# Performance work log

Hardware: AMD Instinct MI355X
Metric: run time of the kernel (lower is better)

Reference implementation:

```python
import jax, jax.numpy as jnp
import numpy as np

ALPHA = 1.0


def setup_inputs() -> dict:
    key = jax.random.key(0)
    k1, k2 = jax.random.split(key)
    x = jax.random.normal(k1, (131072, 512), dtype=jnp.float32)
    # glorot_uniform-ish small init for cluster centers (K, D)
    limit = np.sqrt(6.0 / (128 + 512)).astype(np.float32)
    clusters = jax.random.uniform(k2, (128, 512), dtype=jnp.float32,
                                  minval=-limit, maxval=limit)
    return {"x": x, "clusters": clusters}


def reference(x, clusters):
    # Squared euclidean distance via matmul decomposition:
    # ||x_i - c_j||^2 = ||x_i||^2 + ||c_j||^2 - 2 x_i . c_j
    # Avoids materializing the (N, K, D) broadcast intermediate.
    x2 = jnp.sum(x * x, axis=1, keepdims=True)            # (N, 1)
    c2 = jnp.sum(clusters * clusters, axis=1)             # (K,)
    cross = jnp.einsum('nd,kd->nk', x, clusters)          # (N, K)
    d2 = jnp.maximum(x2 + c2[None, :] - 2.0 * cross, 0.0)  # (N, K)
    q = 1.0 / (1.0 + d2 / ALPHA)
    q = q ** ((ALPHA + 1.0) / 2.0)
    q = q / jnp.sum(q, axis=1, keepdims=True)             # row-normalize
    return q
```

## Files before the change

### kernel.cpp

```cpp
#include <hip/hip_runtime.h>
#include <hip/hip_bf16.h>

typedef __bf16 bf16x8 __attribute__((ext_vector_type(8)));
typedef float f32x4 __attribute__((ext_vector_type(4)));

__global__ __launch_bounds__(64)
void prep_clusters(const float* __restrict__ c, __bf16* __restrict__ cb,
                   float* __restrict__ c2)
{
    const int row = blockIdx.x;
    const int l = threadIdx.x;
    const float* p = c + row * 512 + l * 8;
    f32x4 u0 = *(const f32x4*)p;
    f32x4 u1 = *(const f32x4*)(p + 4);
    bf16x8 v;
    float s = 0.f;
#pragma unroll
    for (int j = 0; j < 4; ++j) {
        v[j]     = (__bf16)u0[j];
        v[4 + j] = (__bf16)u1[j];
        s += u0[j] * u0[j] + u1[j] * u1[j];
    }
    *(bf16x8*)(cb + row * 512 + l * 8) = v;
#pragma unroll
    for (int off = 32; off >= 1; off >>= 1) s += __shfl_xor(s, off);
    if (l == 0) c2[row] = s;
}

__global__ __launch_bounds__(256, 2)
void cluster_q_mfma(const float* __restrict__ x,
                    const __bf16* __restrict__ cb,
                    const float* __restrict__ c2,
                    float* __restrict__ out)
{
    __shared__ float lds[16 * 512];
    __shared__ float rsx[4][16];

    const int tid = threadIdx.x;
    const int l = tid & 63;
    const int w = tid >> 6;
    const int m = l & 15;
    const int g = l >> 4;
    const long brow = (long)blockIdx.x * 256;

    float c2v[2];
#pragma unroll
    for (int nb = 0; nb < 2; ++nb) c2v[nb] = c2[w * 32 + nb * 16 + m];

    bf16x8 bR[2][16];
#pragma unroll
    for (int nb = 0; nb < 2; ++nb)
#pragma unroll
        for (int ks = 0; ks < 16; ++ks)
            bR[nb][ks] = *(const bf16x8*)(
                cb + (w * 32 + nb * 16 + m) * 512 + ks * 32 + g * 8);

    int cow[4];
#pragma unroll
    for (int q = 0; q < 4; ++q)
        cow[q] = (l & 56) + ((l & 7) ^ ((w * 4 + q) & 7));

    const int rbo0 = m * 2048 + (((2 * g)     ^ (m & 7)) * 16);
    const int rbo1 = m * 2048 + (((2 * g + 1) ^ (m & 7)) * 16);

    f32x4 G[8];

#define SB __builtin_amdgcn_sched_barrier(0)
#define GLOAD(P)                                                          \
    { _Pragma("unroll")                                                   \
      for (int i_ = 0; i_ < 8; ++i_)                                      \
          G[i_] = *(const f32x4*)(x + (brow + (long)(P) * 16              \
                     + w * 4 + (i_ >> 1)) * 512 + (i_ & 1) * 256 + l * 4); }
#define DSWRITE()                                                         \
    { _Pragma("unroll")                                                   \
      for (int i_ = 0; i_ < 8; ++i_)                                      \
          *(f32x4*)(&lds[(w * 4 + (i_ >> 1)) * 512 + (i_ & 1) * 256       \
                         + cow[i_ >> 1] * 4]) = G[i_]; }

    GLOAD(0);
    asm volatile("s_waitcnt vmcnt(0)" ::: "memory");
    DSWRITE();
    asm volatile("s_waitcnt lgkmcnt(0)" ::: "memory");
    __builtin_amdgcn_s_barrier();

#pragma unroll 1
    for (int p = 0; p < 16; ++p) {
        if (p < 15) { GLOAD(p + 1); }
        SB;

        f32x4 acc[2] = {f32x4{0.f, 0.f, 0.f, 0.f}, f32x4{0.f, 0.f, 0.f, 0.f}};
        float x2p = 0.f;
        const char* L = (const char*)&lds[0];
#pragma unroll
        for (int ks = 0; ks < 16; ++ks) {
            f32x4 u0 = *(const f32x4*)(L + rbo0 + ks * 128);
            f32x4 u1 = *(const f32x4*)(L + rbo1 + ks * 128);
            bf16x8 aF;
#pragma unroll
            for (int j = 0; j < 4; ++j) {
                aF[j]     = (__bf16)u0[j];
                aF[4 + j] = (__bf16)u1[j];
                x2p += u0[j] * u0[j] + u1[j] * u1[j];
            }
            acc[0] = __builtin_amdgcn_mfma_f32_16x16x32_bf16(aF, bR[0][ks], acc[0], 0, 0, 0);
            acc[1] = __builtin_amdgcn_mfma_f32_16x16x32_bf16(aF, bR[1][ks], acc[1], 0, 0, 0);
        }

        x2p += __shfl_xor(x2p, 16);
        x2p += __shfl_xor(x2p, 32);

        float x2r[4], rs[4];
#pragma unroll
        for (int r = 0; r < 4; ++r) {
            x2r[r] = __shfl(x2p, g * 4 + r);
            rs[r] = 0.f;
        }
#pragma unroll
        for (int nb = 0; nb < 2; ++nb)
#pragma unroll
            for (int r = 0; r < 4; ++r) {
                float d2 = fmaxf(x2r[r] + c2v[nb] - 2.f * acc[nb][r], 0.f);
                float qv = __builtin_amdgcn_rcpf(1.f + d2);
                acc[nb][r] = qv;
                rs[r] += qv;
            }
#pragma unroll
        for (int r = 0; r < 4; ++r) {
            rs[r] += __shfl_xor(rs[r], 1);
            rs[r] += __shfl_xor(rs[r], 2);
            rs[r] += __shfl_xor(rs[r], 4);
            rs[r] += __shfl_xor(rs[r], 8);
        }
        if (m == 0) {
#pragma unroll
            for (int r = 0; r < 4; ++r) rsx[w][g * 4 + r] = rs[r];
        }
        asm volatile("s_waitcnt lgkmcnt(0)" ::: "memory");
        __builtin_amdgcn_s_barrier();

        const long orow = brow + p * 16 + g * 4;
#pragma unroll
        for (int r = 0; r < 4; ++r) {
            const int row16 = g * 4 + r;
            const float inv = __builtin_amdgcn_rcpf(
                rsx[0][row16] + rsx[1][row16] + rsx[2][row16] + rsx[3][row16]);
#pragma unroll
            for (int nb = 0; nb < 2; ++nb)
                out[(orow + r) * 128 + w * 32 + nb * 16 + m] = acc[nb][r] * inv;
        }

        if (p < 15) {
            asm volatile("s_waitcnt vmcnt(8)" ::: "memory");
            SB;
            DSWRITE();
            asm volatile("s_waitcnt lgkmcnt(0)" ::: "memory");
            __builtin_amdgcn_s_barrier();
        }
    }
#undef GLOAD
#undef DSWRITE
#undef SB
}

extern "C" void kernel_launch(void* const* d_in, const int* in_sizes, int n_in,
                              void* d_out, int out_size, void* d_ws, size_t ws_size,
                              hipStream_t stream)
{
    const float* x = (const float*)d_in[0];
    const float* c = (const float*)d_in[1];
    float* out = (float*)d_out;

    float*  c2ws = (float*)d_ws;
    __bf16* cbws = (__bf16*)((char*)d_ws + 1024);

    hipLaunchKernelGGL(prep_clusters, dim3(128), dim3(64), 0, stream, c, cbws, c2ws);

    const int N = in_sizes[0] / 512;
    dim3 grid(N / 256), block(256);
    hipLaunchKernelGGL(cluster_q_mfma, grid, block, 0, stream, x, cbws, c2ws, out);
}
```

Baseline: 82.21 us.

## Double-buffer LDS tiles and prefetch two passes ahead with row-contiguous loads

Switches the x staging tile to a double-buffered LDS layout with two register sets, so global loads are issued two passes ahead while the current buffer is consumed. The global load mapping becomes row-contiguous across 128 threads, with a matching XOR swizzle, and the row-sum scratch is transposed for a single vector read. The goal is to hide HBM latency in this bandwidth-bound kernel. The cost is doubled LDS and register use, which may hurt occupancy, plus redundant loads of the last tile.

```diff
diff --git a/kernel.cpp b/kernel.cpp
--- a/kernel.cpp
+++ b/kernel.cpp
@@ -33,8 +33,8 @@
                     const float* __restrict__ c2,
                     float* __restrict__ out)
 {
-    __shared__ float lds[16 * 512];
-    __shared__ float rsx[4][16];
+    __shared__ float lds[2][16 * 512];
+    __shared__ float rsx[16][4];
 
     const int tid = threadIdx.x;
     const int l = tid & 63;
@@ -55,108 +55,116 @@
             bR[nb][ks] = *(const bf16x8*)(
                 cb + (w * 32 + nb * 16 + m) * 512 + ks * 32 + g * 8);
 
-    int cow[4];
-#pragma unroll
-    for (int q = 0; q < 4; ++q)
-        cow[q] = (l & 56) + ((l & 7) ^ ((w * 4 + q) & 7));
+    const int t7 = tid >> 7;
+    const int ck = tid & 127;
+    const float* gbase = x + (brow + t7) * 512 + ck * 4;
 
     const int rbo0 = m * 2048 + (((2 * g)     ^ (m & 7)) * 16);
     const int rbo1 = m * 2048 + (((2 * g + 1) ^ (m & 7)) * 16);
 
-    f32x4 G[8];
+    f32x4 GA[8], GB[8];
 
 #define SB __builtin_amdgcn_sched_barrier(0)
-#define GLOAD(P)                                                          \
+#define GLOAD(G, P)                                                       \
     { _Pragma("unroll")                                                   \
       for (int i_ = 0; i_ < 8; ++i_)                                      \
-          G[i_] = *(const f32x4*)(x + (brow + (long)(P) * 16              \
-                     + w * 4 + (i_ >> 1)) * 512 + (i_ & 1) * 256 + l * 4); }
-#define DSWRITE()                                                         \
+          G[i_] = *(const f32x4*)(gbase + (long)((P) * 16 + i_ * 2) * 512); }
+#define DSWRITE(BUF, G)                                                   \
     { _Pragma("unroll")                                                   \
-      for (int i_ = 0; i_ < 8; ++i_)                                      \
-          *(f32x4*)(&lds[(w * 4 + (i_ >> 1)) * 512 + (i_ & 1) * 256       \
-                         + cow[i_ >> 1] * 4]) = G[i_]; }
+      for (int i_ = 0; i_ < 8; ++i_) {                                    \
+          const int row_l = i_ * 2 + t7;                                  \
+          *(f32x4*)(&lds[BUF][row_l * 512 + (ck ^ (row_l & 7)) * 4]) = G[i_]; \
+      } }
 
-    GLOAD(0);
+    GLOAD(GA, 0);
     asm volatile("s_waitcnt vmcnt(0)" ::: "memory");
-    DSWRITE();
+    DSWRITE(0, GA);
+    GLOAD(GA, 1);
     asm volatile("s_waitcnt lgkmcnt(0)" ::: "memory");
     __builtin_amdgcn_s_barrier();
 
+#define PASS_BODY(P, BUF, GR, GI)                                         \
+    {                                                                     \
+        const int Pn = ((P) + 2 < 16) ? (P) + 2 : 15;                     \
+        GLOAD(GI, Pn);             \
+        SB;                                                               \
+        f32x4 acc[2] = {f32x4{0.f,0.f,0.f,0.f}, f32x4{0.f,0.f,0.f,0.f}};  \
+        float x2p = 0.f;                                                  \
+        const char* L = (const char*)&lds[BUF][0];                        \
+        _Pragma("unroll")                                                 \
+        for (int ks = 0; ks < 16; ++ks) {                                 \
+            f32x4 u0 = *(const f32x4*)(L + rbo0 + ks * 128);              \
+            f32x4 u1 = *(const f32x4*)(L + rbo1 + ks * 128);              \
+            bf16x8 aF;                                                    \
+            _Pragma("unroll")                                             \
+            for (int j = 0; j < 4; ++j) {                                 \
+                aF[j]     = (__bf16)u0[j];                                \
+                aF[4 + j] = (__bf16)u1[j];                                \
+                x2p += u0[j] * u0[j] + u1[j] * u1[j];                     \
+            }                                                             \
+            acc[0] = __builtin_amdgcn_mfma_f32_16x16x32_bf16(aF, bR[0][ks], acc[0], 0, 0, 0); \
+            acc[1] = __builtin_amdgcn_mfma_f32_16x16x32_bf16(aF, bR[1][ks], acc[1], 0, 0, 0); \
+        }                                                                 \
+        x2p += __shfl_xor(x2p, 16);                                       \
+        x2p += __shfl_xor(x2p, 32);                                       \
+        float x2r[4], rs[4];                                              \
+        _Pragma("unroll")                                                 \
+        for (int r = 0; r < 4; ++r) {                                     \
+            x2r[r] = __shfl(x2p, g * 4 + r);                              \
+            rs[r] = 0.f;                                                  \
+        }                                                                 \
+        _Pragma("unroll")                                                 \
+        for (int nb = 0; nb < 2; ++nb)                                    \
+            _Pragma("unroll")                                             \
+            for (int r = 0; r < 4; ++r) {                                 \
+                float d2 = fmaxf(x2r[r] + c2v[nb] - 2.f * acc[nb][r], 0.f); \
+                float qv = __builtin_amdgcn_rcpf(1.f + d2);               \
+                acc[nb][r] = qv;                                          \
+                rs[r] += qv;                                              \
+            }                                                             \
+        _Pragma("unroll")                                                 \
+        for (int r = 0; r < 4; ++r) {                                     \
+            rs[r] += __shfl_xor(rs[r], 1);                                \
+            rs[r] += __shfl_xor(rs[r], 2);                                \
+            rs[r] += __shfl_xor(rs[r], 4);                                \
+            rs[r] += __shfl_xor(rs[r], 8);                                \
+        }                                                                 \
+        if (m == 0) {                                                     \
+            _Pragma("unroll")                                             \
+            for (int r = 0; r < 4; ++r) rsx[g * 4 + r][w] = rs[r];        \
+        }                                                                 \
+        asm volatile("s_waitcnt lgkmcnt(0)" ::: "memory");                \
+        __builtin_amdgcn_s_barrier();                   \
+        float inv[4];                                                     \
+        _Pragma("unroll")                                                 \
+        for (int r = 0; r < 4; ++r) {                                     \
+            f32x4 v = *(const f32x4*)&rsx[g * 4 + r][0];                  \
+            inv[r] = __builtin_amdgcn_rcpf(v[0] + v[1] + v[2] + v[3]);    \
+        }                                                                 \
+        const long orow = brow + (P) * 16 + g * 4;                        \
+        _Pragma("unroll")                                                 \
+        for (int r = 0; r < 4; ++r)                                       \
+            _Pragma("unroll")                                             \
+            for (int nb = 0; nb < 2; ++nb)                                \
+                out[(orow + r) * 128 + w * 32 + nb * 16 + m] =            \
+                    acc[nb][r] * inv[r];                                  \
+        SB;                                                               \
+        if ((P) < 15) {                                                   \
+            asm volatile("s_waitcnt vmcnt(16)" ::: "memory");  \
+            SB;                                                           \
+            DSWRITE((BUF) ^ 1, GR);                                       \
+            asm volatile("s_waitcnt lgkmcnt(0)" ::: "memory");            \
+            __builtin_amdgcn_s_barrier();       \
+            SB;                                                           \
+        }                                                                 \
+    }
+
 #pragma unroll 1
-    for (int p = 0; p < 16; ++p) {
-        if (p < 15) { GLOAD(p + 1); }
-        SB;
-
-        f32x4 acc[2] = {f32x4{0.f, 0.f, 0.f, 0.f}, f32x4{0.f, 0.f, 0.f, 0.f}};
-        float x2p = 0.f;
-        const char* L = (const char*)&lds[0];
-#pragma unroll
-        for (int ks = 0; ks < 16; ++ks) {
-            f32x4 u0 = *(const f32x4*)(L + rbo0 + ks * 128);
-            f32x4 u1 = *(const f32x4*)(L + rbo1 + ks * 128);
-            bf16x8 aF;
-#pragma unroll
-            for (int j = 0; j < 4; ++j) {
-                aF[j]     = (__bf16)u0[j];
-                aF[4 + j] = (__bf16)u1[j];
-                x2p += u0[j] * u0[j] + u1[j] * u1[j];
-            }
-            acc[0] = __builtin_amdgcn_mfma_f32_16x16x32_bf16(aF, bR[0][ks], acc[0], 0, 0, 0);
-            acc[1] = __builtin_amdgcn_mfma_f32_16x16x32_bf16(aF, bR[1][ks], acc[1], 0, 0, 0);
-        }
-
-        x2p += __shfl_xor(x2p, 16);
-        x2p += __shfl_xor(x2p, 32);
-
-        float x2r[4], rs[4];
-#pragma unroll
-        for (int r = 0; r < 4; ++r) {
-            x2r[r] = __shfl(x2p, g * 4 + r);
-            rs[r] = 0.f;
-        }
-#pragma unroll
-        for (int nb = 0; nb < 2; ++nb)
-#pragma unroll
-            for (int r = 0; r < 4; ++r) {
-                float d2 = fmaxf(x2r[r] + c2v[nb] - 2.f * acc[nb][r], 0.f);
-                float qv = __builtin_amdgcn_rcpf(1.f + d2);
-                acc[nb][r] = qv;
-                rs[r] += qv;
-            }
-#pragma unroll
-        for (int r = 0; r < 4; ++r) {
-            rs[r] += __shfl_xor(rs[r], 1);
-            rs[r] += __shfl_xor(rs[r], 2);
-            rs[r] += __shfl_xor(rs[r], 4);
-            rs[r] += __shfl_xor(rs[r], 8);
-        }
-        if (m == 0) {
-#pragma unroll
-            for (int r = 0; r < 4; ++r) rsx[w][g * 4 + r] = rs[r];
-        }
-        asm volatile("s_waitcnt lgkmcnt(0)" ::: "memory");
-        __builtin_amdgcn_s_barrier();
-
-        const long orow = brow + p * 16 + g * 4;
-#pragma unroll
-        for (int r = 0; r < 4; ++r) {
-            const int row16 = g * 4 + r;
-            const float inv = __builtin_amdgcn_rcpf(
-                rsx[0][row16] + rsx[1][row16] + rsx[2][row16] + rsx[3][row16]);
-#pragma unroll
-            for (int nb = 0; nb < 2; ++nb)
-                out[(orow + r) * 128 + w * 32 + nb * 16 + m] = acc[nb][r] * inv;
-        }
-
-        if (p < 15) {
-            asm volatile("s_waitcnt vmcnt(8)" ::: "memory");
-            SB;
-            DSWRITE();
-            asm volatile("s_waitcnt lgkmcnt(0)" ::: "memory");
-            __builtin_amdgcn_s_barrier();
-        }
+    for (int pp = 0; pp < 8; ++pp) {
+        PASS_BODY(2 * pp,     0, GA, GB);
+        PASS_BODY(2 * pp + 1, 1, GB, GA);
     }
+#undef PASS_BODY
 #undef GLOAD
 #undef DSWRITE
 #undef SB
```

Measured after the change: 87.96 us. +7.0%, slower.

## Use 512-thread blocks with two-deep x prefetch and LDS-staged coalesced output

Applied to the files above, without the earlier changes.

Each block now runs 8 waves, each owning 16 clusters instead of 32. This halves per-wave B-fragment registers and raises the target occupancy. The x tile load is reshaped for 512 threads and the prefetch is issued two tiles ahead, with the LDS write of the next tile overlapped with the normalization stage. Output rows are staged through an LDS transpose buffer and written as coalesced nontemporal float4 stores. In exchange, every wave re-reads and re-converts the full x tile from LDS, doubling LDS read and x² work, and each iteration needs one extra barrier.

```diff
diff --git a/kernel.cpp b/kernel.cpp
--- a/kernel.cpp
+++ b/kernel.cpp
@@ -27,14 +27,15 @@
     if (l == 0) c2[row] = s;
 }
 
-__global__ __launch_bounds__(256, 2)
+__global__ __launch_bounds__(512, 4)
 void cluster_q_mfma(const float* __restrict__ x,
                     const __bf16* __restrict__ cb,
                     const float* __restrict__ c2,
                     float* __restrict__ out)
 {
     __shared__ float lds[16 * 512];
-    __shared__ float rsx[4][16];
+    __shared__ float rsx[8][16];
+    __shared__ float qt[16][132];
 
     const int tid = threadIdx.x;
     const int l = tid & 63;
@@ -43,52 +44,45 @@
     const int g = l >> 4;
     const long brow = (long)blockIdx.x * 256;
 
-    float c2v[2];
+    const float c2v = c2[w * 16 + m];
+
+    bf16x8 bR[16];
 #pragma unroll
-    for (int nb = 0; nb < 2; ++nb) c2v[nb] = c2[w * 32 + nb * 16 + m];
+    for (int ks = 0; ks < 16; ++ks)
+        bR[ks] = *(const bf16x8*)(cb + (w * 16 + m) * 512 + ks * 32 + g * 8);
 
-    bf16x8 bR[2][16];
-#pragma unroll
-    for (int nb = 0; nb < 2; ++nb)
-#pragma unroll
-        for (int ks = 0; ks < 16; ++ks)
-            bR[nb][ks] = *(const bf16x8*)(
-                cb + (w * 32 + nb * 16 + m) * 512 + ks * 32 + g * 8);
-
-    int cow[4];
-#pragma unroll
-    for (int q = 0; q < 4; ++q)
-        cow[q] = (l & 56) + ((l & 7) ^ ((w * 4 + q) & 7));
+    const int t7 = tid >> 7;
+    const int ck = tid & 127;
 
     const int rbo0 = m * 2048 + (((2 * g)     ^ (m & 7)) * 16);
     const int rbo1 = m * 2048 + (((2 * g + 1) ^ (m & 7)) * 16);
 
-    f32x4 G[8];
+    f32x4 G[4];
 
 #define SB __builtin_amdgcn_sched_barrier(0)
 #define GLOAD(P)                                                          \
     { _Pragma("unroll")                                                   \
-      for (int i_ = 0; i_ < 8; ++i_)                                      \
+      for (int i_ = 0; i_ < 4; ++i_)                                      \
           G[i_] = *(const f32x4*)(x + (brow + (long)(P) * 16              \
-                     + w * 4 + (i_ >> 1)) * 512 + (i_ & 1) * 256 + l * 4); }
+                     + i_ * 4 + t7) * 512 + ck * 4); }
 #define DSWRITE()                                                         \
     { _Pragma("unroll")                                                   \
-      for (int i_ = 0; i_ < 8; ++i_)                                      \
-          *(f32x4*)(&lds[(w * 4 + (i_ >> 1)) * 512 + (i_ & 1) * 256       \
-                         + cow[i_ >> 1] * 4]) = G[i_]; }
+      for (int i_ = 0; i_ < 4; ++i_) {                                    \
+          const int row_l = i_ * 4 + t7;                                  \
+          const int swc = (ck & ~7) | ((ck & 7) ^ (row_l & 7));           \
+          *(f32x4*)(&lds[row_l * 512 + swc * 4]) = G[i_];                 \
+      } }
 
     GLOAD(0);
     asm volatile("s_waitcnt vmcnt(0)" ::: "memory");
     DSWRITE();
+    GLOAD(1);
     asm volatile("s_waitcnt lgkmcnt(0)" ::: "memory");
     __builtin_amdgcn_s_barrier();
 
 #pragma unroll 1
     for (int p = 0; p < 16; ++p) {
-        if (p < 15) { GLOAD(p + 1); }
-        SB;
-
-        f32x4 acc[2] = {f32x4{0.f, 0.f, 0.f, 0.f}, f32x4{0.f, 0.f, 0.f, 0.f}};
+        f32x4 acc = f32x4{0.f, 0.f, 0.f, 0.f};
         float x2p = 0.f;
         const char* L = (const char*)&lds[0];
 #pragma unroll
@@ -102,13 +96,11 @@
                 aF[4 + j] = (__bf16)u1[j];
                 x2p += u0[j] * u0[j] + u1[j] * u1[j];
             }
-            acc[0] = __builtin_amdgcn_mfma_f32_16x16x32_bf16(aF, bR[0][ks], acc[0], 0, 0, 0);
-            acc[1] = __builtin_amdgcn_mfma_f32_16x16x32_bf16(aF, bR[1][ks], acc[1], 0, 0, 0);
+            acc = __builtin_amdgcn_mfma_f32_16x16x32_bf16(aF, bR[ks], acc, 0, 0, 0);
         }
 
         x2p += __shfl_xor(x2p, 16);
         x2p += __shfl_xor(x2p, 32);
-
         float x2r[4], rs[4];
 #pragma unroll
         for (int r = 0; r < 4; ++r) {
@@ -116,14 +108,12 @@
             rs[r] = 0.f;
         }
 #pragma unroll
-        for (int nb = 0; nb < 2; ++nb)
-#pragma unroll
-            for (int r = 0; r < 4; ++r) {
-                float d2 = fmaxf(x2r[r] + c2v[nb] - 2.f * acc[nb][r], 0.f);
-                float qv = __builtin_amdgcn_rcpf(1.f + d2);
-                acc[nb][r] = qv;
-                rs[r] += qv;
-            }
+        for (int r = 0; r < 4; ++r) {
+            float d2 = fmaxf(x2r[r] + c2v - 2.f * acc[r], 0.f);
+            float qv = __builtin_amdgcn_rcpf(1.f + d2);
+            acc[r] = qv;
+            rs[r] += qv;
+        }
 #pragma unroll
         for (int r = 0; r < 4; ++r) {
             rs[r] += __shfl_xor(rs[r], 1);
@@ -135,27 +125,44 @@
 #pragma unroll
             for (int r = 0; r < 4; ++r) rsx[w][g * 4 + r] = rs[r];
         }
+
         asm volatile("s_waitcnt lgkmcnt(0)" ::: "memory");
         __builtin_amdgcn_s_barrier();
+        SB;
 
-        const long orow = brow + p * 16 + g * 4;
+        if (p < 15) {
+            if (p == 0) { asm volatile("s_waitcnt vmcnt(0)" ::: "memory"); }
+            else        { asm volatile("s_waitcnt vmcnt(1)" ::: "memory"); }
+            SB;
+            DSWRITE();
+            if (p < 14) { GLOAD(p + 2); }
+        }
+
+        float inv[4];
 #pragma unroll
         for (int r = 0; r < 4; ++r) {
             const int row16 = g * 4 + r;
-            const float inv = __builtin_amdgcn_rcpf(
-                rsx[0][row16] + rsx[1][row16] + rsx[2][row16] + rsx[3][row16]);
+            float s = rsx[0][row16] + rsx[1][row16] + rsx[2][row16] +
+                      rsx[3][row16] + rsx[4][row16] + rsx[5][row16] +
+                      rsx[6][row16] + rsx[7][row16];
+            inv[r] = __builtin_amdgcn_rcpf(s);
+        }
 #pragma unroll
-            for (int nb = 0; nb < 2; ++nb)
-                out[(orow + r) * 128 + w * 32 + nb * 16 + m] = acc[nb][r] * inv;
+        for (int r = 0; r < 4; ++r)
+            qt[g * 4 + r][w * 16 + m] = acc[r] * inv[r];
+
+        asm volatile("s_waitcnt lgkmcnt(0)" ::: "memory");
+        __builtin_amdgcn_s_barrier();
+        SB;
+
+        {
+            const int row = tid >> 5;
+            const int cc = tid & 31;
+            f32x4 v = *(const f32x4*)&qt[row][cc * 4];
+            __builtin_nontemporal_store(
+                v, (f32x4*)(out + (brow + p * 16 + row) * 128 + cc * 4));
         }
-
-        if (p < 15) {
-            asm volatile("s_waitcnt vmcnt(8)" ::: "memory");
-            SB;
-            DSWRITE();
-            asm volatile("s_waitcnt lgkmcnt(0)" ::: "memory");
-            __builtin_amdgcn_s_barrier();
-        }
+        SB;
     }
 #undef GLOAD
 #undef DSWRITE
@@ -176,6 +183,6 @@
     hipLaunchKernelGGL(prep_clusters, dim3(128), dim3(64), 0, stream, c, cbws, c2ws);
 
     const int N = in_sizes[0] / 512;
-    dim3 grid(N / 256), block(256);
+    dim3 grid(N / 256), block(512);
     hipLaunchKernelGGL(cluster_q_mfma, grid, block, 0, stream, x, cbws, c2ws, out);
 }
```

Result: slower. 124.2 us (+51.1%).
